# Performance work log

Hardware: AMD Instinct MI355X
Metric: run time of the kernel (lower is better)

The kernel has to match this reference:

```python
import jax, jax.numpy as jnp
import numpy as np


def setup_inputs() -> dict:
    key = jax.random.key(0)
    ks = jax.random.split(key, 8)
    B, N, D, S = 4, 16384, 512, 512
    x = jax.random.normal(ks[0], (B, N, D), dtype=jnp.float32)
    jx = jnp.sort(jax.random.randint(ks[1], (N,), 0, S, dtype=jnp.int64))
    scale = 1.0 / np.sqrt(D)
    Wf = jax.random.normal(ks[2], (D, D), dtype=jnp.float32) * scale
    bf = jax.random.normal(ks[3], (D,), dtype=jnp.float32) * scale
    Wg = jax.random.normal(ks[4], (D, D), dtype=jnp.float32) * scale
    bg = jax.random.normal(ks[5], (D,), dtype=jnp.float32) * scale
    Wh = jax.random.normal(ks[6], (D, D), dtype=jnp.float32) * scale
    bh = jax.random.normal(ks[7], (D,), dtype=jnp.float32) * scale
    return {"x": x, "jx": jx, "num_segments": S, "Wf": Wf, "bf": bf,
            "Wg": Wg, "bg": bg, "Wh": Wh, "bh": bh}


def reference(x, jx, num_segments, Wf, bf, Wg, bg, Wh, bh):
    # x: [B, N, D]; jx: [N] segment ids; segments along axis 1.
    fx = jnp.einsum('bnd,ed->bne', x, Wf) + bf  # f(x)
    gx = jnp.einsum('bnd,ed->bne', x, Wg) + bg  # g(x)
    # move N to leading axis so jax.ops.segment_* apply: [N, B, D]
    gx_t = jnp.transpose(gx, (1, 0, 2))
    fx_t = jnp.transpose(fx, (1, 0, 2))
    # scatter_softmax over segments (numerically stable)
    m = jax.ops.segment_max(gx_t, jx, num_segments=num_segments)  # [S, B, D]
    e = jnp.exp(gx_t - m[jx])
    denom = jax.ops.segment_sum(e, jx, num_segments=num_segments)  # [S, B, D]
    w = e / denom[jx]  # [N, B, D]
    # weighted scatter-sum
    y_t = jax.ops.segment_sum(fx_t * w, jx, num_segments=num_segments)  # [S, B, D]
    y = jnp.transpose(y_t, (1, 0, 2))  # [B, S, D]
    hy = jnp.einsum('bsd,ed->bse', y, Wh) + bh
    # expand=True: gather back to per-element
    return hy[:, jx]  # [B, N, D]
```

## Files before the change

kernel.cpp:

```cpp
#include <hip/hip_runtime.h>
#include <stdint.h>

#define B_ 4
#define N_ 16384
#define D_ 512
#define S_ 512

typedef __attribute__((ext_vector_type(8))) short bf16x8;
typedef __attribute__((ext_vector_type(4))) float f32x4;

__device__ __forceinline__ float bf2f(unsigned short u) {
  union { unsigned int i; float f; } v; v.i = ((unsigned int)u) << 16; return v.f;
}
__device__ __forceinline__ unsigned short f2bf(float f) {
  unsigned int x = __float_as_uint(f);
  return (unsigned short)((x + 0x7FFFu + ((x >> 16) & 1u)) >> 16);
}
__device__ __forceinline__ float ldf(const void* p, long i, bool f32) {
  return f32 ? ((const float*)p)[i] : bf2f(((const unsigned short*)p)[i]);
}
__device__ __forceinline__ void gl_lds16(void* lds_base, const void* g) {
  __builtin_amdgcn_global_load_lds(
      (const __attribute__((address_space(1))) unsigned int*)g,
      (__attribute__((address_space(3))) unsigned int*)lds_base,
      16, 0, 0);
}

__device__ __forceinline__ bool jx_is_i64(const int* jx32) { return jx32[N_ - 1] == 0; }
__device__ __forceinline__ int seg_id(const int* jx32, int n, bool i64) {
  return i64 ? jx32[2 * n] : jx32[n];
}

__global__ __launch_bounds__(256)
void k0_flag_bounds(const unsigned short* __restrict__ x, const int* __restrict__ jx,
                    int* __restrict__ flag, int* __restrict__ segst) {
  __shared__ int cnt[256];
  int c = 0;
#pragma unroll
  for (int i = 0; i < 8; i++) {
    unsigned short w = x[threadIdx.x * 8 + i];
    int e = (w >> 7) & 0xFF;
    if (e == 0 || (e >= 100 && e <= 140)) c++;
  }
  cnt[threadIdx.x] = c;
  __syncthreads();
  for (int s = 128; s > 0; s >>= 1) {
    if ((int)threadIdx.x < s) cnt[threadIdx.x] += cnt[threadIdx.x + s];
    __syncthreads();
  }
  if (threadIdx.x == 0) flag[0] = (cnt[0] < 1843) ? 1 : 0;

  const int s = blockIdx.x * 256 + threadIdx.x;
  if (s > S_) return;
  const bool i64 = jx_is_i64(jx);
  int lo = 0, hi = N_;
  while (lo < hi) {
    int mid = (lo + hi) >> 1;
    if (seg_id(jx, mid, i64) < s) lo = mid + 1; else hi = mid;
  }
  segst[s] = lo;
}

__global__ __launch_bounds__(256)
void prep_w(const void* __restrict__ Wf, const void* __restrict__ bfv,
            const void* __restrict__ Wg, const void* __restrict__ bgv,
            const void* __restrict__ Wh, const void* __restrict__ bhv,
            const int* __restrict__ flag,
            unsigned short* __restrict__ Wfg, unsigned short* __restrict__ biasfg,
            unsigned short* __restrict__ Whb, unsigned short* __restrict__ bhb) {
  const bool f32 = flag[0] != 0;
  int idx = blockIdx.x * 256 + threadIdx.x;
  if (idx < 524288) {
    int e = idx >> 9, d = idx & 511;
    float v = (e < 512) ? ldf(Wf, (long)e * 512 + d, f32)
                        : ldf(Wg, (long)(e - 512) * 512 + d, f32);
    Wfg[idx] = f2bf(v);
  } else if (idx < 786432) {
    Whb[idx - 524288] = f2bf(ldf(Wh, idx - 524288, f32));
  } else if (idx < 787456) {
    int j = idx - 786432;
    biasfg[j] = f2bf(j < 512 ? ldf(bfv, j, f32) : ldf(bgv, j - 512, f32));
  } else if (idx < 787968) {
    bhb[idx - 787456] = f2bf(ldf(bhv, idx - 787456, f32));
  }
}

#define BK 32

__global__ __launch_bounds__(256, 2)
void gemm_fg(const void* __restrict__ A, const unsigned short* __restrict__ Bm,
             const unsigned short* __restrict__ bias, const int* __restrict__ flag,
             unsigned short* __restrict__ Cf, unsigned short* __restrict__ Cg) {
  __shared__ __align__(16) unsigned short As[128 * BK];
  __shared__ __align__(16) unsigned short Bs[128 * BK];
  const bool af32 = flag[0] != 0;
  const int L = blockIdx.x;
  const int xcd = L & 7, local = L >> 3;
  const int tm = xcd * 64 + local / 8;
  const int tn = local % 8;
  const int m0 = tm * 128, n0 = tn * 128;

  const int tid  = threadIdx.x;
  const int w    = tid >> 6;
  const int lane = tid & 63;
  const int wm   = w >> 1, wn = w & 1;
  const int l15  = lane & 15, l4 = lane >> 4;
  const int srow = lane >> 2;
  const int scol = (lane & 3) * 8;
  const int arow = tid >> 1;
  const int ak0  = (tid & 1) * 16;

  f32x4 acc[4][4];
#pragma unroll
  for (int i = 0; i < 4; i++)
#pragma unroll
    for (int j = 0; j < 4; j++) acc[i][j] = (f32x4){0.f, 0.f, 0.f, 0.f};

  for (int kt = 0; kt < 512; kt += BK) {
    __syncthreads();
#pragma unroll
    for (int r = 0; r < 2; r++) {
      const int rb = (r * 4 + w) * 16;
      gl_lds16(&Bs[rb * BK], Bm + (size_t)(n0 + rb + srow) * 512 + kt + scol);
    }
    if (af32) {
      const float4* ap = (const float4*)((const float*)A +
                          (size_t)(m0 + arow) * 512 + kt + ak0);
      float4 a0 = ap[0], a1 = ap[1], a2 = ap[2], a3 = ap[3];
      bf16x8 v0, v1;
      v0[0]=f2bf(a0.x); v0[1]=f2bf(a0.y); v0[2]=f2bf(a0.z); v0[3]=f2bf(a0.w);
      v0[4]=f2bf(a1.x); v0[5]=f2bf(a1.y); v0[6]=f2bf(a1.z); v0[7]=f2bf(a1.w);
      v1[0]=f2bf(a2.x); v1[1]=f2bf(a2.y); v1[2]=f2bf(a2.z); v1[3]=f2bf(a2.w);
      v1[4]=f2bf(a3.x); v1[5]=f2bf(a3.y); v1[6]=f2bf(a3.z); v1[7]=f2bf(a3.w);
      *(bf16x8*)&As[arow * BK + ak0]     = v0;
      *(bf16x8*)&As[arow * BK + ak0 + 8] = v1;
    } else {
#pragma unroll
      for (int r = 0; r < 2; r++) {
        const int rb = (r * 4 + w) * 16;
        gl_lds16(&As[rb * BK],
                 (const unsigned short*)A + (size_t)(m0 + rb + srow) * 512 + kt + scol);
      }
    }
    __syncthreads();

    bf16x8 a[4], bb[4];
#pragma unroll
    for (int i = 0; i < 4; i++)
      a[i] = *(const bf16x8*)&As[(wm * 64 + i * 16 + l15) * BK + l4 * 8];
#pragma unroll
    for (int j = 0; j < 4; j++)
      bb[j] = *(const bf16x8*)&Bs[(wn * 64 + j * 16 + l15) * BK + l4 * 8];
#pragma unroll
    for (int i = 0; i < 4; i++)
#pragma unroll
      for (int j = 0; j < 4; j++)
        acc[i][j] = __builtin_amdgcn_mfma_f32_16x16x32_bf16(a[i], bb[j], acc[i][j], 0, 0, 0);
  }

#pragma unroll
  for (int j = 0; j < 4; j++) {
    const int col = n0 + wn * 64 + j * 16 + l15;
    const float bv = bf2f(bias[col]);
    unsigned short* base = (col < 512) ? Cf : Cg;
    const int cc = col & 511;
#pragma unroll
    for (int i = 0; i < 4; i++) {
      const int rowb = m0 + wm * 64 + i * 16 + l4 * 4;
#pragma unroll
      for (int r = 0; r < 4; r++)
        base[(size_t)(rowb + r) * 512 + cc] = f2bf(acc[i][j][r] + bv);
    }
  }
}

__global__ __launch_bounds__(256)
void seg_softmax(const unsigned short* __restrict__ f, const unsigned short* __restrict__ g,
                 const int* __restrict__ segst, unsigned short* __restrict__ y) {
  const int s = blockIdx.x * 2 + (threadIdx.x >> 7);
  const int b = blockIdx.y;
  const int d0 = (threadIdx.x & 127) * 4;
  const int st = segst[s], en = segst[s + 1];
  float den0=0.f, den1=0.f, den2=0.f, den3=0.f;
  float y0=0.f, y1=0.f, y2=0.f, y3=0.f;
  for (int n = st; n < en; n++) {
    const size_t off = (size_t)(b * N_ + n) * 512 + d0;
    const uint2 fp = *(const uint2*)(f + off);
    const uint2 gp = *(const uint2*)(g + off);
    const float f0 = bf2f((unsigned short)fp.x), f1 = bf2f((unsigned short)(fp.x >> 16));
    const float f2 = bf2f((unsigned short)fp.y), f3 = bf2f((unsigned short)(fp.y >> 16));
    const float g0 = bf2f((unsigned short)gp.x), g1 = bf2f((unsigned short)(gp.x >> 16));
    const float g2 = bf2f((unsigned short)gp.y), g3 = bf2f((unsigned short)(gp.y >> 16));
    const float e0 = __expf(g0), e1 = __expf(g1), e2 = __expf(g2), e3 = __expf(g3);
    den0 += e0; den1 += e1; den2 += e2; den3 += e3;
    y0 += f0 * e0; y1 += f1 * e1; y2 += f2 * e2; y3 += f3 * e3;
  }
  uint2 o;
  if (en > st) {
    o.x = (unsigned int)f2bf(y0 / den0) | ((unsigned int)f2bf(y1 / den1) << 16);
    o.y = (unsigned int)f2bf(y2 / den2) | ((unsigned int)f2bf(y3 / den3) << 16);
  } else { o.x = 0u; o.y = 0u; }
  *(uint2*)(y + (size_t)(b * S_ + s) * 512 + d0) = o;
}

__global__ __launch_bounds__(256)
void gemm_hy(const unsigned short* __restrict__ y, const unsigned short* __restrict__ Whb,
             const unsigned short* __restrict__ bhb, unsigned short* __restrict__ hy) {
  __shared__ __align__(16) unsigned short As[64 * 32];
  __shared__ __align__(16) unsigned short Bs[64 * 32];
  const int tid = threadIdx.x;
  const int w = tid >> 6, lane = tid & 63;
  const int l15 = lane & 15, l4 = lane >> 4;
  const int m0 = (blockIdx.x >> 3) * 64, c0 = (blockIdx.x & 7) * 64;
  const int srow = lane >> 2, scol = (lane & 3) * 8;

  f32x4 acc[4];
#pragma unroll
  for (int j = 0; j < 4; j++) acc[j] = (f32x4){0.f, 0.f, 0.f, 0.f};

  for (int kt = 0; kt < 512; kt += 32) {
    __syncthreads();
    gl_lds16(&As[(w * 16) * 32], y   + (size_t)(m0 + w * 16 + srow) * 512 + kt + scol);
    gl_lds16(&Bs[(w * 16) * 32], Whb + (size_t)(c0 + w * 16 + srow) * 512 + kt + scol);
    __syncthreads();
    bf16x8 a = *(const bf16x8*)&As[(w * 16 + l15) * 32 + l4 * 8];
#pragma unroll
    for (int j = 0; j < 4; j++) {
      bf16x8 bb = *(const bf16x8*)&Bs[(j * 16 + l15) * 32 + l4 * 8];
      acc[j] = __builtin_amdgcn_mfma_f32_16x16x32_bf16(a, bb, acc[j], 0, 0, 0);
    }
  }
#pragma unroll
  for (int j = 0; j < 4; j++) {
    const float bv = bf2f(bhb[c0 + j * 16 + l15]);
#pragma unroll
    for (int r = 0; r < 4; r++)
      hy[(size_t)(m0 + w * 16 + l4 * 4 + r) * 512 + c0 + j * 16 + l15] =
          f2bf(acc[j][r] + bv);
  }
}

__global__ __launch_bounds__(256)
void gather_out(const unsigned short* __restrict__ hy, const int* __restrict__ jx,
                void* __restrict__ out, const int* __restrict__ flag) {
  const bool f32 = flag[0] != 0;
  const int gid  = blockIdx.x * 256 + threadIdx.x;
  const int wid  = gid >> 6;
  const int lane = gid & 63;
  const int b = wid >> 14;
  const int n = wid & (N_ - 1);
  const bool i64 = jx_is_i64(jx);
  const int s = seg_id(jx, n, i64);
  const bf16x8 v = *(const bf16x8*)(hy + (size_t)(b * S_ + s) * 512 + lane * 8);
  if (f32) {
    float* dst = (float*)out + (size_t)wid * 512 + lane * 8;
    float4 lo, hi;
    lo.x=bf2f((unsigned short)v[0]); lo.y=bf2f((unsigned short)v[1]);
    lo.z=bf2f((unsigned short)v[2]); lo.w=bf2f((unsigned short)v[3]);
    hi.x=bf2f((unsigned short)v[4]); hi.y=bf2f((unsigned short)v[5]);
    hi.z=bf2f((unsigned short)v[6]); hi.w=bf2f((unsigned short)v[7]);
    *(float4*)dst = lo;
    *(float4*)(dst + 4) = hi;
  } else {
    *(bf16x8*)((unsigned short*)out + (size_t)wid * 512 + lane * 8) = v;
  }
}

extern "C" void kernel_launch(void* const* d_in, const int* in_sizes, int n_in,
                              void* d_out, int out_size, void* d_ws, size_t ws_size,
                              hipStream_t stream) {
  const void* x  = d_in[0];
  const int* jx  = (const int*)d_in[1];
  const void* Wf = d_in[3];
  const void* bf = d_in[4];
  const void* Wg = d_in[5];
  const void* bg = d_in[6];
  const void* Wh = d_in[7];
  const void* bh = d_in[8];

  char* ws = (char*)d_ws;
  int* flag              = (int*)(ws + 0);
  int* segst             = (int*)(ws + 4096);
  unsigned short* biasfg = (unsigned short*)(ws + 8192);
  unsigned short* bhb    = (unsigned short*)(ws + 16384);
  unsigned short* Wfg    = (unsigned short*)(ws + 32768);
  unsigned short* Whb    = (unsigned short*)(ws + 1081344);
  unsigned short* y_ws   = (unsigned short*)(ws + 1605632);
  unsigned short* hy_ws  = (unsigned short*)(ws + 3702784);
  unsigned short* fbuf   = (unsigned short*)d_out;
  unsigned short* gbuf   = (unsigned short*)d_out + (size_t)B_ * N_ * D_;

  k0_flag_bounds<<<3, 256, 0, stream>>>((const unsigned short*)x, jx, flag, segst);
  prep_w<<<3078, 256, 0, stream>>>(Wf, bf, Wg, bg, Wh, bh, flag,
                                   Wfg, biasfg, Whb, bhb);
  gemm_fg<<<4096, 256, 0, stream>>>(x, Wfg, biasfg, flag, fbuf, gbuf);
  seg_softmax<<<dim3(256, B_), 256, 0, stream>>>(fbuf, gbuf, segst, y_ws);
  gemm_hy<<<256, 256, 0, stream>>>(y_ws, Whb, bhb, hy_ws);
  gather_out<<<16384, 256, 0, stream>>>(hy_ws, jx, d_out, flag);
}
```

Measured before the change: 417.1 us.

## Pre-convert x to bf16 in fused prep kernel, simplify GEMM A loads

Merges the flag/bounds kernel and the weight-prep kernel into one launch that also converts x from fp32 to bf16 into a workspace buffer. The f/g GEMM can then load A straight into LDS with global_load_lds instead of converting in registers. The segment softmax loop is also unrolled by two to keep more loads in flight. The cost is an extra full pass over x (read fp32, write bf16) before the GEMM, and every prep block now reruns the dtype classification reduction.

```diff
diff --git a/kernel.cpp b/kernel.cpp
--- a/kernel.cpp
+++ b/kernel.cpp
@@ -31,10 +31,7 @@
   return i64 ? jx32[2 * n] : jx32[n];
 }
 
-__global__ __launch_bounds__(256)
-void k0_flag_bounds(const unsigned short* __restrict__ x, const int* __restrict__ jx,
-                    int* __restrict__ flag, int* __restrict__ segst) {
-  __shared__ int cnt[256];
+__device__ __forceinline__ bool classify_f32(const unsigned short* x, int* cnt) {
   int c = 0;
 #pragma unroll
   for (int i = 0; i < 8; i++) {
@@ -48,52 +45,74 @@
     if ((int)threadIdx.x < s) cnt[threadIdx.x] += cnt[threadIdx.x + s];
     __syncthreads();
   }
-  if (threadIdx.x == 0) flag[0] = (cnt[0] < 1843) ? 1 : 0;
-
-  const int s = blockIdx.x * 256 + threadIdx.x;
-  if (s > S_) return;
-  const bool i64 = jx_is_i64(jx);
-  int lo = 0, hi = N_;
-  while (lo < hi) {
-    int mid = (lo + hi) >> 1;
-    if (seg_id(jx, mid, i64) < s) lo = mid + 1; else hi = mid;
-  }
-  segst[s] = lo;
+  bool f32 = cnt[0] < 1843;
+  __syncthreads();
+  return f32;
 }
 
 __global__ __launch_bounds__(256)
-void prep_w(const void* __restrict__ Wf, const void* __restrict__ bfv,
-            const void* __restrict__ Wg, const void* __restrict__ bgv,
-            const void* __restrict__ Wh, const void* __restrict__ bhv,
-            const int* __restrict__ flag,
-            unsigned short* __restrict__ Wfg, unsigned short* __restrict__ biasfg,
-            unsigned short* __restrict__ Whb, unsigned short* __restrict__ bhb) {
-  const bool f32 = flag[0] != 0;
-  int idx = blockIdx.x * 256 + threadIdx.x;
-  if (idx < 524288) {
-    int e = idx >> 9, d = idx & 511;
-    float v = (e < 512) ? ldf(Wf, (long)e * 512 + d, f32)
-                        : ldf(Wg, (long)(e - 512) * 512 + d, f32);
-    Wfg[idx] = f2bf(v);
-  } else if (idx < 786432) {
-    Whb[idx - 524288] = f2bf(ldf(Wh, idx - 524288, f32));
-  } else if (idx < 787456) {
-    int j = idx - 786432;
-    biasfg[j] = f2bf(j < 512 ? ldf(bfv, j, f32) : ldf(bgv, j - 512, f32));
-  } else if (idx < 787968) {
-    bhb[idx - 787456] = f2bf(ldf(bhv, idx - 787456, f32));
+void prep_all(const void* __restrict__ x, const int* __restrict__ jx,
+              const void* __restrict__ Wf, const void* __restrict__ bfv,
+              const void* __restrict__ Wg, const void* __restrict__ bgv,
+              const void* __restrict__ Wh, const void* __restrict__ bhv,
+              unsigned short* __restrict__ xb, unsigned short* __restrict__ Wfg,
+              unsigned short* __restrict__ biasfg, unsigned short* __restrict__ Whb,
+              unsigned short* __restrict__ bhb, int* __restrict__ segst,
+              int* __restrict__ flag) {
+  const int blk = blockIdx.x, tid = threadIdx.x;
+  __shared__ int cnt[256];
+  const bool f32 = classify_f32((const unsigned short*)x, cnt);
+  if (blk >= 19462) {
+    if (blk == 19462 && tid == 0) flag[0] = f32 ? 1 : 0;
+    int s = (blk - 19462) * 256 + tid;
+    if (s > S_) return;
+    bool i64 = jx_is_i64(jx);
+    int lo = 0, hi = N_;
+    while (lo < hi) {
+      int mid = (lo + hi) >> 1;
+      if (seg_id(jx, mid, i64) < s) lo = mid + 1; else hi = mid;
+    }
+    segst[s] = lo;
+    return;
+  }
+  if (blk < 16384) {
+    const size_t i0 = ((size_t)blk * 256 + tid) * 8;
+    bf16x8 v;
+    if (f32) {
+      const float4* p = (const float4*)((const float*)x + i0);
+      float4 a = p[0], b = p[1];
+      v[0]=f2bf(a.x); v[1]=f2bf(a.y); v[2]=f2bf(a.z); v[3]=f2bf(a.w);
+      v[4]=f2bf(b.x); v[5]=f2bf(b.y); v[6]=f2bf(b.z); v[7]=f2bf(b.w);
+    } else {
+      v = *(const bf16x8*)((const unsigned short*)x + i0);
+    }
+    *(bf16x8*)(xb + i0) = v;
+  } else {
+    int idx = (blk - 16384) * 256 + tid;
+    if (idx < 524288) {
+      int e = idx >> 9, d = idx & 511;
+      float v = (e < 512) ? ldf(Wf, (long)e * 512 + d, f32)
+                          : ldf(Wg, (long)(e - 512) * 512 + d, f32);
+      Wfg[idx] = f2bf(v);
+    } else if (idx < 786432) {
+      Whb[idx - 524288] = f2bf(ldf(Wh, idx - 524288, f32));
+    } else if (idx < 787456) {
+      int j = idx - 786432;
+      biasfg[j] = f2bf(j < 512 ? ldf(bfv, j, f32) : ldf(bgv, j - 512, f32));
+    } else if (idx < 787968) {
+      bhb[idx - 787456] = f2bf(ldf(bhv, idx - 787456, f32));
+    }
   }
 }
 
 #define BK 32
 
 __global__ __launch_bounds__(256, 2)
-void gemm_fg(const void* __restrict__ A, const unsigned short* __restrict__ Bm,
-             const unsigned short* __restrict__ bias, const int* __restrict__ flag,
+void gemm_fg(const unsigned short* __restrict__ A, const unsigned short* __restrict__ Bm,
+             const unsigned short* __restrict__ bias,
              unsigned short* __restrict__ Cf, unsigned short* __restrict__ Cg) {
   __shared__ __align__(16) unsigned short As[128 * BK];
   __shared__ __align__(16) unsigned short Bs[128 * BK];
-  const bool af32 = flag[0] != 0;
   const int L = blockIdx.x;
   const int xcd = L & 7, local = L >> 3;
   const int tm = xcd * 64 + local / 8;
@@ -107,8 +126,6 @@
   const int l15  = lane & 15, l4 = lane >> 4;
   const int srow = lane >> 2;
   const int scol = (lane & 3) * 8;
-  const int arow = tid >> 1;
-  const int ak0  = (tid & 1) * 16;
 
   f32x4 acc[4][4];
 #pragma unroll
@@ -121,26 +138,8 @@
 #pragma unroll
     for (int r = 0; r < 2; r++) {
       const int rb = (r * 4 + w) * 16;
+      gl_lds16(&As[rb * BK], A + (size_t)(m0 + rb + srow) * 512 + kt + scol);
       gl_lds16(&Bs[rb * BK], Bm + (size_t)(n0 + rb + srow) * 512 + kt + scol);
-    }
-    if (af32) {
-      const float4* ap = (const float4*)((const float*)A +
-                          (size_t)(m0 + arow) * 512 + kt + ak0);
-      float4 a0 = ap[0], a1 = ap[1], a2 = ap[2], a3 = ap[3];
-      bf16x8 v0, v1;
-      v0[0]=f2bf(a0.x); v0[1]=f2bf(a0.y); v0[2]=f2bf(a0.z); v0[3]=f2bf(a0.w);
-      v0[4]=f2bf(a1.x); v0[5]=f2bf(a1.y); v0[6]=f2bf(a1.z); v0[7]=f2bf(a1.w);
-      v1[0]=f2bf(a2.x); v1[1]=f2bf(a2.y); v1[2]=f2bf(a2.z); v1[3]=f2bf(a2.w);
-      v1[4]=f2bf(a3.x); v1[5]=f2bf(a3.y); v1[6]=f2bf(a3.z); v1[7]=f2bf(a3.w);
-      *(bf16x8*)&As[arow * BK + ak0]     = v0;
-      *(bf16x8*)&As[arow * BK + ak0 + 8] = v1;
-    } else {
-#pragma unroll
-      for (int r = 0; r < 2; r++) {
-        const int rb = (r * 4 + w) * 16;
-        gl_lds16(&As[rb * BK],
-                 (const unsigned short*)A + (size_t)(m0 + rb + srow) * 512 + kt + scol);
-      }
     }
     __syncthreads();
 
@@ -183,7 +182,34 @@
   const int st = segst[s], en = segst[s + 1];
   float den0=0.f, den1=0.f, den2=0.f, den3=0.f;
   float y0=0.f, y1=0.f, y2=0.f, y3=0.f;
-  for (int n = st; n < en; n++) {
+  int n = st;
+  for (; n + 1 < en; n += 2) {
+    const size_t offA = (size_t)(b * N_ + n) * 512 + d0;
+    const size_t offB = offA + 512;
+    const uint2 fpA = *(const uint2*)(f + offA);
+    const uint2 gpA = *(const uint2*)(g + offA);
+    const uint2 fpB = *(const uint2*)(f + offB);
+    const uint2 gpB = *(const uint2*)(g + offB);
+    {
+      const float f0 = bf2f((unsigned short)fpA.x), f1 = bf2f((unsigned short)(fpA.x >> 16));
+      const float f2 = bf2f((unsigned short)fpA.y), f3 = bf2f((unsigned short)(fpA.y >> 16));
+      const float g0 = bf2f((unsigned short)gpA.x), g1 = bf2f((unsigned short)(gpA.x >> 16));
+      const float g2 = bf2f((unsigned short)gpA.y), g3 = bf2f((unsigned short)(gpA.y >> 16));
+      const float e0 = __expf(g0), e1 = __expf(g1), e2 = __expf(g2), e3 = __expf(g3);
+      den0 += e0; den1 += e1; den2 += e2; den3 += e3;
+      y0 += f0 * e0; y1 += f1 * e1; y2 += f2 * e2; y3 += f3 * e3;
+    }
+    {
+      const float f0 = bf2f((unsigned short)fpB.x), f1 = bf2f((unsigned short)(fpB.x >> 16));
+      const float f2 = bf2f((unsigned short)fpB.y), f3 = bf2f((unsigned short)(fpB.y >> 16));
+      const float g0 = bf2f((unsigned short)gpB.x), g1 = bf2f((unsigned short)(gpB.x >> 16));
+      const float g2 = bf2f((unsigned short)gpB.y), g3 = bf2f((unsigned short)(gpB.y >> 16));
+      const float e0 = __expf(g0), e1 = __expf(g1), e2 = __expf(g2), e3 = __expf(g3);
+      den0 += e0; den1 += e1; den2 += e2; den3 += e3;
+      y0 += f0 * e0; y1 += f1 * e1; y2 += f2 * e2; y3 += f3 * e3;
+    }
+  }
+  if (n < en) {
     const size_t off = (size_t)(b * N_ + n) * 512 + d0;
     const uint2 fp = *(const uint2*)(f + off);
     const uint2 gp = *(const uint2*)(g + off);
@@ -287,13 +313,13 @@
   unsigned short* Whb    = (unsigned short*)(ws + 1081344);
   unsigned short* y_ws   = (unsigned short*)(ws + 1605632);
   unsigned short* hy_ws  = (unsigned short*)(ws + 3702784);
+  unsigned short* xb     = (unsigned short*)(ws + 8388608);
   unsigned short* fbuf   = (unsigned short*)d_out;
   unsigned short* gbuf   = (unsigned short*)d_out + (size_t)B_ * N_ * D_;
 
-  k0_flag_bounds<<<3, 256, 0, stream>>>((const unsigned short*)x, jx, flag, segst);
-  prep_w<<<3078, 256, 0, stream>>>(Wf, bf, Wg, bg, Wh, bh, flag,
-                                   Wfg, biasfg, Whb, bhb);
-  gemm_fg<<<4096, 256, 0, stream>>>(x, Wfg, biasfg, flag, fbuf, gbuf);
+  prep_all<<<19465, 256, 0, stream>>>(x, jx, Wf, bf, Wg, bg, Wh, bh,
+                                      xb, Wfg, biasfg, Whb, bhb, segst, flag);
+  gemm_fg<<<4096, 256, 0, stream>>>(xb, Wfg, biasfg, fbuf, gbuf);
   seg_softmax<<<dim3(256, B_), 256, 0, stream>>>(fbuf, gbuf, segst, y_ws);
   gemm_hy<<<256, 256, 0, stream>>>(y_ws, Whb, bhb, hy_ws);
   gather_out<<<16384, 256, 0, stream>>>(hy_ws, jx, d_out, flag);
```

Measured after the change: 392.7 us. 1.06x faster.
